# Optimization experiments

Hardware: AMD Instinct MI355X
Metric: run time of the kernel (lower is better)

## Reference

```python
import jax, jax.numpy as jnp
import numpy as np
import math

SCALES = (0.25, 0.125, 0.0625, 0.03125)
CANONICAL_SIZE = 20.0
OUT_SIZE = (5, 5, 5)
SAMPLING_RATIO = 2


def _trilinear(f, pts):
    # f: [C, D0, D1, D2]; pts: [P, 3] in feature-map coords. Returns [C, P].
    Df = jnp.asarray(f.shape[1:], pts.dtype)
    Di = jnp.asarray(f.shape[1:], jnp.int32)
    # ROIAlign convention: samples with any coord < -1 or > D contribute 0.
    valid = jnp.all((pts > -1.0) & (pts < Df), axis=-1)  # [P]
    p = jnp.clip(pts, 0.0, Df - 1.0)
    p0 = jnp.floor(p)
    fr = p - p0                                  # [P,3]
    i0 = p0.astype(jnp.int32)
    i1 = jnp.minimum(i0 + 1, Di - 1)
    w = jnp.stack([1.0 - fr, fr], 0)             # [2,P,3]
    ii = jnp.stack([i0, i1], 0)                  # [2,P,3]
    acc = jnp.zeros((f.shape[0], pts.shape[0]), f.dtype)
    for a in (0, 1):
        for b in (0, 1):
            for c in (0, 1):
                wgt = w[a, :, 0] * w[b, :, 1] * w[c, :, 2]        # [P]
                val = f[:, ii[a, :, 0], ii[b, :, 1], ii[c, :, 2]]  # [C,P]
                acc = acc + val * wgt[None, :]
    return acc * valid[None, :].astype(f.dtype)


def _axis_samples(n, sr):
    # normalized sub-sample centers in (0,1), flattened bin-major: [n*sr]
    bins = jnp.arange(n, dtype=jnp.float32)
    sub = (jnp.arange(sr, dtype=jnp.float32) + 0.5) / sr
    return ((bins[:, None] + sub[None, :]) / n).reshape(-1)


def _pool_one(feats, bidx, roi7, scale):
    # feats: [B,C,D0,D1,D2]; roi7 = [c0,c1,c2,s0,s1,s2,angle_deg]
    f = feats[bidx]                              # [C,D0,D1,D2]
    ctr = roi7[0:3] * scale
    size = roi7[3:6] * scale
    theta = roi7[6] * (math.pi / 180.0)          # pooler op converts deg -> rad
    os0, os1, os2 = OUT_SIZE
    sr = SAMPLING_RATIO
    g0 = (_axis_samples(os0, sr) - 0.5) * size[0]
    g1 = (_axis_samples(os1, sr) - 0.5) * size[1]
    g2 = (_axis_samples(os2, sr) - 0.5) * size[2]
    O0, O1, O2 = jnp.meshgrid(g0, g1, g2, indexing='ij')
    c, s = jnp.cos(theta), jnp.sin(theta)
    # rotation in the (axis0, axis1) plane of the permuted roi coords
    r0 = c * O0 - s * O1
    r1 = s * O0 + c * O1
    pts = jnp.stack([ctr[0] + r0, ctr[1] + r1, ctr[2] + O2], -1)  # [os0*sr,os1*sr,os2*sr,3]
    sampled = _trilinear(f, pts.reshape(-1, 3))                    # [C, P]
    C = f.shape[0]
    sampled = sampled.reshape(C, os0, sr, os1, sr, os2, sr)
    return sampled.mean(axis=(2, 4, 6))          # [C, os0, os1, os2]


def setup_inputs() -> dict:
    key = jax.random.key(0)
    k = jax.random.split(key, 10)
    B, C, R = 2, 64, 128
    x0 = jax.random.normal(k[0], (B, C, 64, 64, 64), jnp.float32)
    x1 = jax.random.normal(k[1], (B, C, 32, 32, 32), jnp.float32)
    x2 = jax.random.normal(k[2], (B, C, 16, 16, 16), jnp.float32)
    x3 = jax.random.normal(k[3], (B, C, 8, 8, 8), jnp.float32)
    ctr = jax.random.uniform(k[4], (R, 3), jnp.float32, 20.0, 236.0)
    dxy = jax.random.uniform(k[5], (R, 2), jnp.float32, 1.0, 16.0)
    dz = jax.random.uniform(k[6], (R, 1), jnp.float32, 1.0, 8.0)
    theta = jax.random.uniform(k[7], (R, 1), jnp.float32, -math.pi, math.pi)
    bbox3d = jnp.concatenate([ctr, dxy, dz, theta], axis=1)  # standard: [x,y,z,dx,dy,dz,theta]
    batch_ids = jax.random.randint(k[8], (R,), 0, B, jnp.int32)
    return {"x0": x0, "x1": x1, "x2": x2, "x3": x3, "bbox3d": bbox3d, "batch_ids": batch_ids}


def reference(x0, x1, x2, x3, bbox3d, batch_ids):
    b = bbox3d
    # convert_to_roi_format: permute [0,2,1,3,5,4,6,7] (drop id col here), angle rad->deg
    roi7 = jnp.stack([b[:, 1], b[:, 0], b[:, 2], b[:, 4], b[:, 3], b[:, 5],
                      b[:, 6] * (180.0 / math.pi)], axis=1)
    # LevelMapper_3d
    size = jnp.sqrt(jnp.maximum(b[:, 3], b[:, 4]))
    rate = size / CANONICAL_SIZE
    levels = jnp.argmin(jnp.abs(jnp.asarray(SCALES, jnp.float32)[None, :] - rate[:, None]), axis=1)
    feats = [x0, x1, x2, x3]
    R, C = roi7.shape[0], x0.shape[1]
    os0, os1, os2 = OUT_SIZE
    result = jnp.zeros((R, C, os0, os1, os2), x0.dtype)
    for l in range(len(SCALES)):
        pooled = jax.vmap(lambda r, bi: _pool_one(feats[l], bi, r, SCALES[l]))(roi7, batch_ids)
        mask = (levels == l)[:, None, None, None, None]
        result = jnp.where(mask, pooled, result)
    return result
```

## Files before the change

kernel.cpp:

```cpp
#include <hip/hip_runtime.h>
#include <math.h>

#define CHB 8
#define C_NUM 64
#define NCELL 125
#define MAX_VOX 256
#define NITEMS 250

__device__ __forceinline__ int swz(int L) { return L ^ ((L >> 3) & 7); }

__device__ __forceinline__ void acc8(const float4* __restrict__ rg4, int v, float w,
                                     float4& A, float4& B) {
    int P = swz(v * 2);
    float4 lo = rg4[P];
    float4 hi = rg4[P ^ 1];
    A.x = fmaf(lo.x, w, A.x); A.y = fmaf(lo.y, w, A.y);
    A.z = fmaf(lo.z, w, A.z); A.w = fmaf(lo.w, w, A.w);
    B.x = fmaf(hi.x, w, B.x); B.y = fmaf(hi.y, w, B.y);
    B.z = fmaf(hi.z, w, B.z); B.w = fmaf(hi.w, w, B.w);
}

__global__ __launch_bounds__(256) void pooler_kernel(
    const float* __restrict__ x0, const float* __restrict__ x1,
    const float* __restrict__ x2, const float* __restrict__ x3,
    const float* __restrict__ bbox, const int* __restrict__ bids,
    float* __restrict__ out)
{
    __shared__ float reg[MAX_VOX * CHB];
    __shared__ float partial[NITEMS * 9];

    const int blk = blockIdx.x;
    const int r   = blk >> 3;
    const int cg  = blk & 7;
    const int tid = threadIdx.x;

    const float b0 = bbox[r*7+0], b1 = bbox[r*7+1], b2 = bbox[r*7+2];
    const float b3 = bbox[r*7+3], b4 = bbox[r*7+4], b5 = bbox[r*7+5];
    const float b6 = bbox[r*7+6];
    const int bid  = bids[r];

    const float rate = sqrtf(fmaxf(b3, b4)) / 20.0f;
    const float SC[4] = {0.25f, 0.125f, 0.0625f, 0.03125f};
    int lvl = 0;
    float best = fabsf(SC[0] - rate);
    #pragma unroll
    for (int j = 1; j < 4; ++j) {
        float d = fabsf(SC[j] - rate);
        if (d < best) { best = d; lvl = j; }
    }
    const float scale = SC[lvl];

    const float* f; int D;
    if (lvl == 0)      { f = x0; D = 64; }
    else if (lvl == 1) { f = x1; D = 32; }
    else if (lvl == 2) { f = x2; D = 16; }
    else               { f = x3; D = 8;  }
    const float Df = (float)D;

    const float ctr0 = b1 * scale;
    const float ctr1 = b0 * scale;
    const float ctr2 = b2 * scale;
    const float sz0  = b4 * scale;
    const float sz1  = b3 * scale;
    const float sz2  = b5 * scale;
    const float theta = (b6 * (180.0f / (float)M_PI)) * ((float)M_PI / 180.0f);
    float st, ct;
    sincosf(theta, &st, &ct);

    const float hx = 0.451f * (fabsf(ct) * sz0 + fabsf(st) * sz1) + 0.01f;
    const float hy = 0.451f * (fabsf(st) * sz0 + fabsf(ct) * sz1) + 0.01f;
    const float hz = 0.451f * sz2 + 0.01f;
    const int x_lo = (int)fminf(fmaxf(ctr0 - hx, 0.0f), Df - 1.0f);
    const int y_lo = (int)fminf(fmaxf(ctr1 - hy, 0.0f), Df - 1.0f);
    const int z_lo = (int)fminf(fmaxf(ctr2 - hz, 0.0f), Df - 1.0f);
    const int x_hi = (int)fminf(fmaxf(ctr0 + hx, 0.0f), Df - 1.0f);
    const int y_hi = (int)fminf(fmaxf(ctr1 + hy, 0.0f), Df - 1.0f);
    const int z_hi = (int)fminf(fmaxf(ctr2 + hz, 0.0f), Df - 1.0f);

    const int nx = min(x_hi - x_lo + 2, D - x_lo);
    const int ny = min(y_hi - y_lo + 2, D - y_lo);
    const int nz = min(z_hi - z_lo + 2, D - z_lo);

    int RX2 = 2; while (RX2 < nx) RX2 <<= 1; RX2 = min(RX2, 8);
    int RY2 = 2; while (RY2 < ny) RY2 <<= 1; RY2 = min(RY2, 8);
    int RZ2 = 2; while (RZ2 < nz) RZ2 <<= 1; RZ2 = min(RZ2, 4);
    const int lz  = __builtin_ctz(RZ2);
    const int ly  = __builtin_ctz(RY2);
    const int lx  = __builtin_ctz(RX2);
    const int sxs = lz + ly;
    const int lnv = lx + ly + lz;
    const int nvox = 1 << lnv;

    const size_t vox = (size_t)D * D * D;
    const float* fbase = f + ((size_t)bid * C_NUM + (size_t)cg * CHB) * vox;
    const int total_e = nvox * CHB;
    for (int e = tid; e < total_e; e += 256) {
        int ch = e >> lnv;
        int v  = e & (nvox - 1);
        int rz = v & (RZ2 - 1);
        int ry = (v >> lz) & (RY2 - 1);
        int rx = v >> sxs;
        int gx = min(x_lo + rx, D - 1);
        int gy = min(y_lo + ry, D - 1);
        int gz = min(z_lo + rz, D - 1);
        float val = fbase[(size_t)ch * vox + (size_t)(gx * D + gy) * D + gz];
        int P = swz(v * 2 + (ch >> 2));
        reg[P * 4 + (ch & 3)] = val;
    }
    __syncthreads();

    if (tid < NITEMS) {
        const int cell  = tid >> 1;
        const int shalf = tid & 1;
        const int i0 = cell / 25;
        const int rem = cell - i0 * 25;
        const int i1 = rem / 5;
        const int i2 = rem - i1 * 5;

        float4 accA = make_float4(0.f, 0.f, 0.f, 0.f);
        float4 accB = make_float4(0.f, 0.f, 0.f, 0.f);
        const float4* rg4 = (const float4*)reg;

        #pragma unroll
        for (int s = 0; s < 4; ++s) {
            const int s0 = shalf, s1 = (s >> 1) & 1, s2 = s & 1;
            float u0 = ((float)i0 + ((float)s0 + 0.5f) * 0.5f) / 5.0f;
            float u1 = ((float)i1 + ((float)s1 + 0.5f) * 0.5f) / 5.0f;
            float u2 = ((float)i2 + ((float)s2 + 0.5f) * 0.5f) / 5.0f;
            float g0 = (u0 - 0.5f) * sz0;
            float g1 = (u1 - 0.5f) * sz1;
            float g2 = (u2 - 0.5f) * sz2;
            float px = ctr0 + (ct * g0 - st * g1);
            float py = ctr1 + (st * g0 + ct * g1);
            float pz = ctr2 + g2;
            float validf = ((px > -1.0f) && (px < Df) &&
                            (py > -1.0f) && (py < Df) &&
                            (pz > -1.0f) && (pz < Df)) ? 1.0f : 0.0f;
            float q0 = fminf(fmaxf(px, 0.0f), Df - 1.0f);
            float q1 = fminf(fmaxf(py, 0.0f), Df - 1.0f);
            float q2 = fminf(fmaxf(pz, 0.0f), Df - 1.0f);
            int A0 = (int)q0, A1 = (int)q1, A2 = (int)q2;
            float f0 = q0 - (float)A0;
            float f1 = q1 - (float)A1;
            float f2 = q2 - (float)A2;
            int d0 = ((A0 + 1 < D) ? 1 : 0) << sxs;
            int d1 = ((A1 + 1 < D) ? 1 : 0) << lz;
            int d2 = (A2 + 1 < D) ? 1 : 0;
            int base = ((A0 - x_lo) << sxs) + ((A1 - y_lo) << lz) + (A2 - z_lo);

            float wx0 = 1.0f - f0, wx1 = f0;
            float wy0 = 1.0f - f1, wy1 = f1;
            float wz0 = (1.0f - f2) * validf, wz1 = f2 * validf;
            float w00 = wx0 * wy0, w01 = wx0 * wy1;
            float w10 = wx1 * wy0, w11 = wx1 * wy1;

            acc8(rg4, base,                w00 * wz0, accA, accB);
            acc8(rg4, base + d2,           w00 * wz1, accA, accB);
            acc8(rg4, base + d1,           w01 * wz0, accA, accB);
            acc8(rg4, base + d1 + d2,      w01 * wz1, accA, accB);
            acc8(rg4, base + d0,           w10 * wz0, accA, accB);
            acc8(rg4, base + d0 + d2,      w10 * wz1, accA, accB);
            acc8(rg4, base + d0 + d1,      w11 * wz0, accA, accB);
            acc8(rg4, base + d0 + d1 + d2, w11 * wz1, accA, accB);
        }

        const int pb = tid * 9;
        partial[pb + 0] = accA.x; partial[pb + 1] = accA.y;
        partial[pb + 2] = accA.z; partial[pb + 3] = accA.w;
        partial[pb + 4] = accB.x; partial[pb + 5] = accB.y;
        partial[pb + 6] = accB.z; partial[pb + 7] = accB.w;
    }
    __syncthreads();

    float4* ob4 = (float4*)(out + (size_t)r * (C_NUM * NCELL) + (size_t)cg * (CHB * NCELL));
    for (int q = tid; q < 250; q += 256) {
        float vres[4];
        #pragma unroll
        for (int j = 0; j < 4; ++j) {
            int o = q * 4 + j;
            unsigned ch = (unsigned)o / 125u;
            int cell = o - (int)ch * 125;
            vres[j] = (partial[(cell * 2) * 9 + ch] +
                       partial[(cell * 2 + 1) * 9 + ch]) * 0.125f;
        }
        ob4[q] = make_float4(vres[0], vres[1], vres[2], vres[3]);
    }
}

extern "C" void kernel_launch(void* const* d_in, const int* in_sizes, int n_in,
                              void* d_out, int out_size, void* d_ws, size_t ws_size,
                              hipStream_t stream) {
    const float* x0   = (const float*)d_in[0];
    const float* x1   = (const float*)d_in[1];
    const float* x2   = (const float*)d_in[2];
    const float* x3   = (const float*)d_in[3];
    const float* bbox = (const float*)d_in[4];
    const int*   bids = (const int*)d_in[5];
    float* out = (float*)d_out;

    hipLaunchKernelGGL(pooler_kernel, dim3(1024), dim3(256), 0, stream,
                       x0, x1, x2, x3, bbox, bids, out);
}
```

Baseline: 188.2 us.

## Halve channels per block to 4 and batch gather loads before LDS stores

Each block now handles 4 channels instead of 8, doubling the grid to 2048 blocks. The LDS layout, accumulators and partial buffer shrink to match. The global gather is split into an unrolled phase that issues all loads into registers before a second phase writes them to shared memory, so memory latency can overlap. The trade-off is that per-block setup (ROI decode, level mapping, sample coordinate and weight computation) is repeated twice as often for the same amount of work.

After: 188.9 us. Within noise of the previous version (+0.4%).

```diff
diff --git a/kernel.cpp b/kernel.cpp
--- a/kernel.cpp
+++ b/kernel.cpp
@@ -1,7 +1,7 @@
 #include <hip/hip_runtime.h>
 #include <math.h>
 
-#define CHB 8
+#define CHB 4
 #define C_NUM 64
 #define NCELL 125
 #define MAX_VOX 256
@@ -9,15 +9,11 @@
 
 __device__ __forceinline__ int swz(int L) { return L ^ ((L >> 3) & 7); }
 
-__device__ __forceinline__ void acc8(const float4* __restrict__ rg4, int v, float w,
-                                     float4& A, float4& B) {
-    int P = swz(v * 2);
-    float4 lo = rg4[P];
-    float4 hi = rg4[P ^ 1];
+__device__ __forceinline__ void acc4(const float4* __restrict__ rg4, int v, float w,
+                                     float4& A) {
+    float4 lo = rg4[swz(v)];
     A.x = fmaf(lo.x, w, A.x); A.y = fmaf(lo.y, w, A.y);
     A.z = fmaf(lo.z, w, A.z); A.w = fmaf(lo.w, w, A.w);
-    B.x = fmaf(hi.x, w, B.x); B.y = fmaf(hi.y, w, B.y);
-    B.z = fmaf(hi.z, w, B.z); B.w = fmaf(hi.w, w, B.w);
 }
 
 __global__ __launch_bounds__(256) void pooler_kernel(
@@ -27,11 +23,11 @@
     float* __restrict__ out)
 {
     __shared__ float reg[MAX_VOX * CHB];
-    __shared__ float partial[NITEMS * 9];
+    __shared__ float partial[NITEMS * 5];
 
     const int blk = blockIdx.x;
-    const int r   = blk >> 3;
-    const int cg  = blk & 7;
+    const int r   = blk >> 4;
+    const int cg  = blk & 15;
     const int tid = threadIdx.x;
 
     const float b0 = bbox[r*7+0], b1 = bbox[r*7+1], b2 = bbox[r*7+2];
@@ -86,26 +82,37 @@
     int RZ2 = 2; while (RZ2 < nz) RZ2 <<= 1; RZ2 = min(RZ2, 4);
     const int lz  = __builtin_ctz(RZ2);
     const int ly  = __builtin_ctz(RY2);
-    const int lx  = __builtin_ctz(RX2);
     const int sxs = lz + ly;
-    const int lnv = lx + ly + lz;
+    const int lnv = __builtin_ctz(RX2) + ly + lz;
     const int nvox = 1 << lnv;
 
     const size_t vox = (size_t)D * D * D;
     const float* fbase = f + ((size_t)bid * C_NUM + (size_t)cg * CHB) * vox;
     const int total_e = nvox * CHB;
-    for (int e = tid; e < total_e; e += 256) {
-        int ch = e >> lnv;
-        int v  = e & (nvox - 1);
-        int rz = v & (RZ2 - 1);
-        int ry = (v >> lz) & (RY2 - 1);
-        int rx = v >> sxs;
-        int gx = min(x_lo + rx, D - 1);
-        int gy = min(y_lo + ry, D - 1);
-        int gz = min(z_lo + rz, D - 1);
-        float val = fbase[(size_t)ch * vox + (size_t)(gx * D + gy) * D + gz];
-        int P = swz(v * 2 + (ch >> 2));
-        reg[P * 4 + (ch & 3)] = val;
+    float vals[4];
+    #pragma unroll
+    for (int i = 0; i < 4; ++i) {
+        int e = tid + (i << 8);
+        if (e < total_e) {
+            int ch = e >> lnv;
+            int v  = e & (nvox - 1);
+            int rz = v & (RZ2 - 1);
+            int ry = (v >> lz) & (RY2 - 1);
+            int rx = v >> sxs;
+            int gx = min(x_lo + rx, D - 1);
+            int gy = min(y_lo + ry, D - 1);
+            int gz = min(z_lo + rz, D - 1);
+            vals[i] = fbase[(size_t)ch * vox + (size_t)(gx * D + gy) * D + gz];
+        }
+    }
+    #pragma unroll
+    for (int i = 0; i < 4; ++i) {
+        int e = tid + (i << 8);
+        if (e < total_e) {
+            int ch = e >> lnv;
+            int v  = e & (nvox - 1);
+            reg[swz(v) * 4 + ch] = vals[i];
+        }
     }
     __syncthreads();
 
@@ -118,7 +125,6 @@
         const int i2 = rem - i1 * 5;
 
         float4 accA = make_float4(0.f, 0.f, 0.f, 0.f);
-        float4 accB = make_float4(0.f, 0.f, 0.f, 0.f);
         const float4* rg4 = (const float4*)reg;
 
         #pragma unroll
@@ -154,34 +160,32 @@
             float w00 = wx0 * wy0, w01 = wx0 * wy1;
             float w10 = wx1 * wy0, w11 = wx1 * wy1;
 
-            acc8(rg4, base,                w00 * wz0, accA, accB);
-            acc8(rg4, base + d2,           w00 * wz1, accA, accB);
-            acc8(rg4, base + d1,           w01 * wz0, accA, accB);
-            acc8(rg4, base + d1 + d2,      w01 * wz1, accA, accB);
-            acc8(rg4, base + d0,           w10 * wz0, accA, accB);
-            acc8(rg4, base + d0 + d2,      w10 * wz1, accA, accB);
-            acc8(rg4, base + d0 + d1,      w11 * wz0, accA, accB);
-            acc8(rg4, base + d0 + d1 + d2, w11 * wz1, accA, accB);
-        }
-
-        const int pb = tid * 9;
+            acc4(rg4, base,                w00 * wz0, accA);
+            acc4(rg4, base + d2,           w00 * wz1, accA);
+            acc4(rg4, base + d1,           w01 * wz0, accA);
+            acc4(rg4, base + d1 + d2,      w01 * wz1, accA);
+            acc4(rg4, base + d0,           w10 * wz0, accA);
+            acc4(rg4, base + d0 + d2,      w10 * wz1, accA);
+            acc4(rg4, base + d0 + d1,      w11 * wz0, accA);
+            acc4(rg4, base + d0 + d1 + d2, w11 * wz1, accA);
+        }
+
+        const int pb = tid * 5;
         partial[pb + 0] = accA.x; partial[pb + 1] = accA.y;
         partial[pb + 2] = accA.z; partial[pb + 3] = accA.w;
-        partial[pb + 4] = accB.x; partial[pb + 5] = accB.y;
-        partial[pb + 6] = accB.z; partial[pb + 7] = accB.w;
     }
     __syncthreads();
 
     float4* ob4 = (float4*)(out + (size_t)r * (C_NUM * NCELL) + (size_t)cg * (CHB * NCELL));
-    for (int q = tid; q < 250; q += 256) {
+    for (int q = tid; q < 125; q += 256) {
         float vres[4];
         #pragma unroll
         for (int j = 0; j < 4; ++j) {
             int o = q * 4 + j;
             unsigned ch = (unsigned)o / 125u;
             int cell = o - (int)ch * 125;
-            vres[j] = (partial[(cell * 2) * 9 + ch] +
-                       partial[(cell * 2 + 1) * 9 + ch]) * 0.125f;
+            vres[j] = (partial[(cell * 2) * 5 + ch] +
+                       partial[(cell * 2 + 1) * 5 + ch]) * 0.125f;
         }
         ob4[q] = make_float4(vres[0], vres[1], vres[2], vres[3]);
     }
@@ -198,6 +202,6 @@
     const int*   bids = (const int*)d_in[5];
     float* out = (float*)d_out;
 
-    hipLaunchKernelGGL(pooler_kernel, dim3(1024), dim3(256), 0, stream,
+    hipLaunchKernelGGL(pooler_kernel, dim3(2048), dim3(256), 0, stream,
                        x0, x1, x2, x3, bbox, bids, out);
 }
```
